# Kernel optimization log

Measured on AMD Instinct MI355X. Metric: run time of the kernel, lower is better.

Reference implementation:

```python
import jax, jax.numpy as jnp
import numpy as np

EPS = 1e-7  # K.epsilon()
ROUTINGS = 3


def squash(s):
    # squash along last axis: s * ||s||^2 / (1 + ||s||^2) / ||s||
    sq_norm = jnp.sum(jnp.square(s), axis=-1, keepdims=True)
    scale = sq_norm / (1.0 + sq_norm) / jnp.sqrt(sq_norm + EPS)
    return scale * s


def setup_inputs() -> dict:
    key = jax.random.key(0)
    k1, k2 = jax.random.split(key)
    B, N, I = 64, 2048, 16      # batch, in_num_capsule, in_capsule_dim
    J, K = 32, 32               # num_capsule, capsule_dim
    inputs = jax.random.normal(k1, (B, N, I), dtype=jnp.float32)
    W = jax.random.normal(k2, (J, N, K, I), dtype=jnp.float32) * 0.05
    return {"inputs": inputs, "W": W}


def reference(inputs, W):
    # u_hat[b,j,n,k] = sum_i inputs[b,n,i] * W[j,n,k,i]
    u_hat = jnp.einsum('bni,jnki->bjnk', inputs, W)
    B, J, N, _ = u_hat.shape
    b = jnp.zeros((B, J, N), dtype=u_hat.dtype)
    outputs = None
    for i in range(ROUTINGS):
        c = jax.nn.softmax(b, axis=1)                       # softmax over num_capsule
        s = jnp.einsum('bjn,bjnk->bjk', c, u_hat)           # weighted sum over in caps
        outputs = squash(s)                                  # [B, J, K]
        if i < ROUTINGS - 1:
            b = b + jnp.einsum('bjk,bjnk->bjn', outputs, u_hat)
    return outputs
```

## Files before the change

kernel.cpp:

```cpp
#include <hip/hip_runtime.h>
#include <hip/hip_bf16.h>

typedef unsigned int  u32;
typedef unsigned short u16;
typedef __attribute__((ext_vector_type(8)))  short short8;
typedef __attribute__((ext_vector_type(16))) float f32x16;

#define B_ 64
#define N_ 2048
#define I_ 16
#define J_ 32
#define K_ 32
#define CH_  32
#define WTOT ((size_t)J_*N_*K_*I_)

__device__ __forceinline__ float bf2f(u16 u){ return __uint_as_float(((u32)u)<<16); }
__device__ __forceinline__ short f2bf(float f){
  __hip_bfloat16 h = __float2bfloat16(f);
  short s; __builtin_memcpy(&s, &h, 2); return s;
}

__global__ __launch_bounds__(256) void detect(const u16* __restrict__ X,
                                              const u16* __restrict__ W,
                                              int* __restrict__ flags)
{
  __shared__ int sx, sw;
  if (threadIdx.x == 0){ sx = 0; sw = 0; }
  __syncthreads();
  int bx = 0, bw = 0;
  for (int i = threadIdx.x; i < 8192; i += 256){
    int ex = (X[2*i] >> 7) & 0xFF;
    int ew = (W[2*i] >> 7) & 0xFF;
    if (ex >= 0x90) bx = 1;
    if (ew >= 0x90) bw = 1;
  }
  if (bx) atomicOr(&sx, 1);
  if (bw) atomicOr(&sw, 1);
  __syncthreads();
  if (threadIdx.x == 0){ flags[0] = sx; flags[1] = sw; }
}

__global__ __launch_bounds__(256) void pack_xw(const void* __restrict__ Xv,
                                               const void* __restrict__ Wv,
                                               const int* __restrict__ flags,
                                               u16* __restrict__ X_p,
                                               u16* __restrict__ W_p)
{
  if (blockIdx.x < 8192){
    const size_t base = ((size_t)blockIdx.x*256 + threadIdx.x)*16;
    if (flags[1]){
      const float4* src = (const float4*)((const float*)Wv + base);
      float4 v0=src[0], v1=src[1], v2=src[2], v3=src[3];
      short8 a, b;
      a[0]=f2bf(v0.x); a[1]=f2bf(v0.y); a[2]=f2bf(v0.z); a[3]=f2bf(v0.w);
      a[4]=f2bf(v1.x); a[5]=f2bf(v1.y); a[6]=f2bf(v1.z); a[7]=f2bf(v1.w);
      b[0]=f2bf(v2.x); b[1]=f2bf(v2.y); b[2]=f2bf(v2.z); b[3]=f2bf(v2.w);
      b[4]=f2bf(v3.x); b[5]=f2bf(v3.y); b[6]=f2bf(v3.z); b[7]=f2bf(v3.w);
      *(short8*)(W_p + base)     = a;
      *(short8*)(W_p + base + 8) = b;
    } else {
      const short8* src = (const short8*)((const u16*)Wv + base);
      *(short8*)(W_p + base)     = src[0];
      *(short8*)(W_p + base + 8) = src[1];
    }
  } else {
    const int bid = blockIdx.x - 8192;
    const int l = threadIdx.x & 63, w = threadIdx.x >> 6;
    const int n = bid*4 + w;
    const bool xf32 = flags[0] != 0;
    const int ih = (l>>5)*8;
    u16 out[16];
    #pragma unroll
    for (int t=0;t<2;++t){
      const int b = t*32 + (l&31);
      if (xf32){
        const float4* xp = (const float4*)((const float*)Xv + ((size_t)b*N_ + n)*I_ + ih);
        float4 v0 = xp[0], v1 = xp[1];
        out[t*8+0]=(u16)f2bf(v0.x); out[t*8+1]=(u16)f2bf(v0.y);
        out[t*8+2]=(u16)f2bf(v0.z); out[t*8+3]=(u16)f2bf(v0.w);
        out[t*8+4]=(u16)f2bf(v1.x); out[t*8+5]=(u16)f2bf(v1.y);
        out[t*8+6]=(u16)f2bf(v1.z); out[t*8+7]=(u16)f2bf(v1.w);
      } else {
        const u16* xp = (const u16*)Xv + ((size_t)b*N_ + n)*I_ + ih;
        #pragma unroll
        for (int q=0;q<8;++q) out[t*8+q] = xp[q];
      }
    }
    u16* dst = X_p + (size_t)n*1024 + l*16;
    short8 s0, s1;
    #pragma unroll
    for (int q=0;q<8;++q){ s0[q]=(short)out[q]; s1[q]=(short)out[8+q]; }
    *(short8*)dst = s0;
    *(short8*)(dst+8) = s1;
  }
}

template<int R>
__global__ __launch_bounds__(256) void accum_kernel(
    const u16* __restrict__ X_p, const u16* __restrict__ W_p,
    const float* __restrict__ c_buf, const float* __restrict__ sumb,
    float* __restrict__ part)
{
  __shared__ float red[4][2048];
  const int l  = threadIdx.x & 63;
  const int w  = threadIdx.x >> 6;
  const int j  = blockIdx.y;
  const int ch = blockIdx.x;
  const int n0 = ch*64 + w*16;
  const int kc = l & 31;
  const int ih = (l >> 5) * 8;

  f32x16 C0, C1;
  #pragma unroll
  for (int r=0;r<16;++r){ C0[r]=0.f; C1[r]=0.f; }

  #pragma unroll 4
  for (int t=0;t<16;++t){
    const int n = n0 + t;
    const u16* xp = X_p + (size_t)n*1024 + l*16;
    short8 xa0 = *(const short8*)xp;
    short8 xa1 = *(const short8*)(xp+8);
    short8 a0, a1;
    if constexpr (R==0){ a0 = xa0; a1 = xa1; }
    else {
      const float iS0 = sumb[(size_t)n*64 + kc];
      const float iS1 = sumb[(size_t)n*64 + 32 + kc];
      const float c0 = iS0 * c_buf[((size_t)n*J_ + j)*64 + kc];
      const float c1 = iS1 * c_buf[((size_t)n*J_ + j)*64 + 32 + kc];
      #pragma unroll
      for (int q=0;q<8;++q){
        a0[q] = f2bf(c0 * bf2f((u16)xa0[q]));
        a1[q] = f2bf(c1 * bf2f((u16)xa1[q]));
      }
    }
    short8 bfr = *(const short8*)(W_p + ((size_t)j*N_ + n)*512 + kc*16 + ih);
    C0 = __builtin_amdgcn_mfma_f32_32x32x16_bf16(a0, bfr, C0, 0,0,0);
    C1 = __builtin_amdgcn_mfma_f32_32x32x16_bf16(a1, bfr, C1, 0,0,0);
  }

  #pragma unroll
  for (int r=0;r<16;++r){
    red[w][r*64 + l]      = C0[r];
    red[w][(16+r)*64 + l] = C1[r];
  }
  __syncthreads();

  float* dst = part + ((size_t)ch*J_ + j)*2048;
  #pragma unroll
  for (int p = threadIdx.x; p < 2048; p += 256)
    dst[p] = red[0][p] + red[1][p] + red[2][p] + red[3][p];
}

template<int SQ>
__global__ __launch_bounds__(256) void reduce_squash(
    const float* __restrict__ part, float* __restrict__ o_t,
    const int* __restrict__ flags, void* __restrict__ d_out)
{
  __shared__ float sacc[2048];
  const int j = blockIdx.x;
  for (int p = threadIdx.x; p < 2048; p += 256){
    float sum = 0.f;
    #pragma unroll 4
    for (int ch=0; ch<CH_; ++ch)
      sum += part[((size_t)ch*J_ + j)*2048 + p];
    const int r  = p >> 6, l = p & 63;
    const int kc = l & 31, h = l >> 5;
    const int rr = r & 15, tile = r >> 4;
    const int b  = tile*32 + (rr&3) + 8*(rr>>2) + 4*h;
    sacc[kc*64 + b] = sum;
  }
  __syncthreads();

  if (threadIdx.x < 64){
    const int b = threadIdx.x;
    float sq = 0.f;
    #pragma unroll
    for (int k=0;k<K_;++k){
      float v = sacc[k*64 + b];
      if constexpr (SQ==0) v *= (1.0f/32.0f);
      sq += v*v;
    }
    const float scale = sq/(1.f+sq)/sqrtf(sq+1e-7f);
    if constexpr (SQ==0){
      #pragma unroll
      for (int k=0;k<K_;++k)
        o_t[((size_t)j*K_ + k)*64 + b] = scale * sacc[k*64+b] * (1.0f/32.0f);
    } else if constexpr (SQ==1){
      #pragma unroll
      for (int k=0;k<K_;++k)
        o_t[((size_t)j*K_ + k)*64 + b] += scale * sacc[k*64+b];
    } else {
      const bool f32o = (flags[0]!=0) && (flags[1]!=0);
      if (f32o){
        float* po = (float*)d_out;
        #pragma unroll
        for (int k=0;k<K_;++k)
          po[(size_t)b*(J_*K_) + j*K_ + k] = scale * sacc[k*64+b];
      } else {
        __hip_bfloat16* po = (__hip_bfloat16*)d_out;
        #pragma unroll
        for (int k=0;k<K_;++k)
          po[(size_t)b*(J_*K_) + j*K_ + k] = __float2bfloat16(scale * sacc[k*64+b]);
      }
    }
  }
}

__global__ __launch_bounds__(256) void logits_kernel(
    const u16* __restrict__ X_p, const u16* __restrict__ W_p,
    const float* __restrict__ o_t, float* __restrict__ c_buf)
{
  const int l  = threadIdx.x & 63;
  const int w  = threadIdx.x >> 6;
  const int j  = blockIdx.y;
  const int n0 = blockIdx.x*32 + w*8;
  const int kc = l & 31;
  const int h  = l >> 5;
  const int ih = h*8;

  float o_r0[16], o_r1[16];
  #pragma unroll
  for (int r=0;r<16;++r){
    const int k = (r&3) + 8*(r>>2) + 4*h;
    o_r0[r] = o_t[((size_t)j*K_ + k)*64 + kc];
    o_r1[r] = o_t[((size_t)j*K_ + k)*64 + 32 + kc];
  }

  #pragma unroll 2
  for (int t=0;t<8;++t){
    const int n = n0 + t;
    const u16* xp = X_p + (size_t)n*1024 + l*16;
    short8 xa0 = *(const short8*)xp;
    short8 xa1 = *(const short8*)(xp+8);
    short8 wfr = *(const short8*)(W_p + ((size_t)j*N_ + n)*512 + kc*16 + ih);
    f32x16 C0, C1;
    #pragma unroll
    for (int r=0;r<16;++r){ C0[r]=0.f; C1[r]=0.f; }
    C0 = __builtin_amdgcn_mfma_f32_32x32x16_bf16(wfr, xa0, C0, 0,0,0);
    C1 = __builtin_amdgcn_mfma_f32_32x32x16_bf16(wfr, xa1, C1, 0,0,0);
    float d0 = 0.f, d1 = 0.f;
    #pragma unroll
    for (int r=0;r<16;++r){ d0 += C0[r]*o_r0[r]; d1 += C1[r]*o_r1[r]; }
    d0 += __shfl_xor(d0, 32, 64);
    d1 += __shfl_xor(d1, 32, 64);
    const float val = (l >= 32) ? d1 : d0;
    c_buf[((size_t)n*J_ + j)*64 + l] = __expf(val);
  }
}

__global__ __launch_bounds__(256) void rowsum(const float* __restrict__ c_buf,
                                              float* __restrict__ sumb)
{
  const int l = threadIdx.x & 63, w = threadIdx.x >> 6;
  const int n = blockIdx.x*4 + w;
  const float* p = c_buf + (size_t)n*J_*64 + l;
  float s = 0.f;
  #pragma unroll
  for (int jj=0;jj<J_;++jj) s += p[jj*64];
  sumb[(size_t)n*64 + l] = 1.0f/s;
}

extern "C" void kernel_launch(void* const* d_in, const int* in_sizes, int n_in,
                              void* d_out, int out_size, void* d_ws, size_t ws_size,
                              hipStream_t stream)
{
  const void* X  = d_in[0];
  const void* Wm = d_in[1];

  float* ws    = (float*)d_ws;
  float* o_t   = ws;
  int*   flags = (int*)(ws + 65536);
  u16*   X_p   = (u16*)(ws + 65536 + 128);
  u16*   W_p   = X_p + (size_t)N_*1024;
  float* c_buf = (float*)(W_p + WTOT);
  float* sumb  = c_buf + (size_t)N_*J_*64;
  float* part  = sumb + (size_t)N_*64;

  const dim3 blk(256);
  const dim3 g_ac(CH_, J_);
  const dim3 g_lg(64,  J_);

  detect<<<1, blk, 0, stream>>>((const u16*)X, (const u16*)Wm, flags);
  pack_xw<<<8192 + N_/4, blk, 0, stream>>>(X, Wm, flags, X_p, W_p);

  accum_kernel<0><<<g_ac, blk, 0, stream>>>(X_p, W_p, nullptr, nullptr, part);
  reduce_squash<0><<<J_, blk, 0, stream>>>(part, o_t, flags, nullptr);

  logits_kernel<<<g_lg, blk, 0, stream>>>(X_p, W_p, o_t, c_buf);
  rowsum<<<N_/4, blk, 0, stream>>>(c_buf, sumb);
  accum_kernel<1><<<g_ac, blk, 0, stream>>>(X_p, W_p, c_buf, sumb, part);
  reduce_squash<1><<<J_, blk, 0, stream>>>(part, o_t, flags, nullptr);

  logits_kernel<<<g_lg, blk, 0, stream>>>(X_p, W_p, o_t, c_buf);
  rowsum<<<N_/4, blk, 0, stream>>>(c_buf, sumb);
  accum_kernel<1><<<g_ac, blk, 0, stream>>>(X_p, W_p, c_buf, sumb, part);
  reduce_squash<2><<<J_, blk, 0, stream>>>(part, o_t, flags, d_out);
}
```

Measured before the change: 381.3 us.

## Parallelize reduce_squash across 256 blocks with wavefront shuffle norm reduction

The reduce_squash kernel moves from 32 blocks, each reducing all 2048 partials and then computing the squash norm with only 64 active threads, to 256 blocks where each thread reduces one partial across the chunks. The squared norm over the 32 k-lanes is now computed with xor shuffles inside a wavefront, which removes the shared-memory staging and the barrier. This spreads a small, latency-bound kernel over more compute units and runs it three times per call. In exchange, the output stores are more scattered.

```diff
diff --git a/kernel.cpp b/kernel.cpp
--- a/kernel.cpp
+++ b/kernel.cpp
@@ -156,52 +156,44 @@
     const float* __restrict__ part, float* __restrict__ o_t,
     const int* __restrict__ flags, void* __restrict__ d_out)
 {
-  __shared__ float sacc[2048];
-  const int j = blockIdx.x;
-  for (int p = threadIdx.x; p < 2048; p += 256){
-    float sum = 0.f;
-    #pragma unroll 4
-    for (int ch=0; ch<CH_; ++ch)
-      sum += part[((size_t)ch*J_ + j)*2048 + p];
-    const int r  = p >> 6, l = p & 63;
-    const int kc = l & 31, h = l >> 5;
-    const int rr = r & 15, tile = r >> 4;
-    const int b  = tile*32 + (rr&3) + 8*(rr>>2) + 4*h;
-    sacc[kc*64 + b] = sum;
-  }
-  __syncthreads();
-
-  if (threadIdx.x < 64){
-    const int b = threadIdx.x;
-    float sq = 0.f;
-    #pragma unroll
-    for (int k=0;k<K_;++k){
-      float v = sacc[k*64 + b];
-      if constexpr (SQ==0) v *= (1.0f/32.0f);
-      sq += v*v;
-    }
-    const float scale = sq/(1.f+sq)/sqrtf(sq+1e-7f);
-    if constexpr (SQ==0){
-      #pragma unroll
-      for (int k=0;k<K_;++k)
-        o_t[((size_t)j*K_ + k)*64 + b] = scale * sacc[k*64+b] * (1.0f/32.0f);
-    } else if constexpr (SQ==1){
-      #pragma unroll
-      for (int k=0;k<K_;++k)
-        o_t[((size_t)j*K_ + k)*64 + b] += scale * sacc[k*64+b];
+  const int j    = blockIdx.x & 31;
+  const int rseg = blockIdx.x >> 5;
+  const int rl   = threadIdx.x >> 6;
+  const int l    = threadIdx.x & 63;
+  const int r    = rseg*4 + rl;
+  const int p    = r*64 + l;
+
+  float sum = 0.f;
+  const float* src = part + (size_t)j*2048 + p;
+  #pragma unroll 8
+  for (int ch=0; ch<CH_; ++ch)
+    sum += src[(size_t)ch*J_*2048];
+
+  const int kc = l & 31, h = l >> 5;
+  const int rr = r & 15, tile = r >> 4;
+  const int b  = tile*32 + (rr&3) + 8*(rr>>2) + 4*h;
+
+  float v = sum;
+  if constexpr (SQ==0) v *= (1.0f/32.0f);
+
+  float sq = v*v;
+  sq += __shfl_xor(sq, 1,  64);
+  sq += __shfl_xor(sq, 2,  64);
+  sq += __shfl_xor(sq, 4,  64);
+  sq += __shfl_xor(sq, 8,  64);
+  sq += __shfl_xor(sq, 16, 64);
+  const float scale = sq/(1.f+sq)/sqrtf(sq+1e-7f);
+
+  if constexpr (SQ==0){
+    o_t[((size_t)j*K_ + kc)*64 + b] = scale * v;
+  } else if constexpr (SQ==1){
+    o_t[((size_t)j*K_ + kc)*64 + b] += scale * v;
+  } else {
+    const bool f32o = (flags[0]!=0) && (flags[1]!=0);
+    if (f32o){
+      ((float*)d_out)[(size_t)b*(J_*K_) + j*K_ + kc] = scale * v;
     } else {
-      const bool f32o = (flags[0]!=0) && (flags[1]!=0);
-      if (f32o){
-        float* po = (float*)d_out;
-        #pragma unroll
-        for (int k=0;k<K_;++k)
-          po[(size_t)b*(J_*K_) + j*K_ + k] = scale * sacc[k*64+b];
-      } else {
-        __hip_bfloat16* po = (__hip_bfloat16*)d_out;
-        #pragma unroll
-        for (int k=0;k<K_;++k)
-          po[(size_t)b*(J_*K_) + j*K_ + k] = __float2bfloat16(scale * sacc[k*64+b]);
-      }
+      ((__hip_bfloat16*)d_out)[(size_t)b*(J_*K_) + j*K_ + kc] = __float2bfloat16(scale * v);
     }
   }
 }
@@ -284,15 +276,15 @@
   pack_xw<<<8192 + N_/4, blk, 0, stream>>>(X, Wm, flags, X_p, W_p);
 
   accum_kernel<0><<<g_ac, blk, 0, stream>>>(X_p, W_p, nullptr, nullptr, part);
-  reduce_squash<0><<<J_, blk, 0, stream>>>(part, o_t, flags, nullptr);
+  reduce_squash<0><<<256, blk, 0, stream>>>(part, o_t, flags, nullptr);
 
   logits_kernel<<<g_lg, blk, 0, stream>>>(X_p, W_p, o_t, c_buf);
   rowsum<<<N_/4, blk, 0, stream>>>(c_buf, sumb);
   accum_kernel<1><<<g_ac, blk, 0, stream>>>(X_p, W_p, c_buf, sumb, part);
-  reduce_squash<1><<<J_, blk, 0, stream>>>(part, o_t, flags, nullptr);
+  reduce_squash<1><<<256, blk, 0, stream>>>(part, o_t, flags, nullptr);
 
   logits_kernel<<<g_lg, blk, 0, stream>>>(X_p, W_p, o_t, c_buf);
   rowsum<<<N_/4, blk, 0, stream>>>(c_buf, sumb);
   accum_kernel<1><<<g_ac, blk, 0, stream>>>(X_p, W_p, c_buf, sumb, part);
-  reduce_squash<2><<<J_, blk, 0, stream>>>(part, o_t, flags, d_out);
-}
+  reduce_squash<2><<<256, blk, 0, stream>>>(part, o_t, flags, d_out);
+}
```

After: 323.3 us. 1.18x faster.
